# Kernel optimization log

Measured on AMD Instinct MI355X. Metric: run time of the kernel, lower is better.

The kernel has to match this reference:

```python
import jax, jax.numpy as jnp
import numpy as np


def _warp3d(img, flow):
    """Faithful port of Warper3d.forward.

    img:  [B, C, D, H, W]
    flow: [B, 3, D, H, W]  (flow[:,0]=x/W disp, flow[:,1]=y/H disp, flow[:,2]=z/D disp)

    The torch module normalizes coords align_corners=True style (2*v/(S-1)-1)
    but calls F.grid_sample with its DEFAULT align_corners=False and
    padding_mode='border'. We replicate exactly that composition.
    """
    B, C, D, H, W = img.shape
    dt = img.dtype
    zz = jnp.arange(D, dtype=dt).reshape(1, D, 1, 1)
    yy = jnp.arange(H, dtype=dt).reshape(1, 1, H, 1)
    xx = jnp.arange(W, dtype=dt).reshape(1, 1, 1, W)

    vx = xx + flow[:, 0]  # [B,D,H,W]
    vy = yy + flow[:, 1]
    vz = zz + flow[:, 2]

    # module's normalization (align_corners=True convention)
    gx = 2.0 * vx / (W - 1) - 1.0
    gy = 2.0 * vy / (H - 1) - 1.0
    gz = 2.0 * vz / (D - 1) - 1.0

    # grid_sample default align_corners=False un-normalization
    ix = ((gx + 1.0) * W - 1.0) * 0.5
    iy = ((gy + 1.0) * H - 1.0) * 0.5
    iz = ((gz + 1.0) * D - 1.0) * 0.5

    # padding_mode='border': clamp sample coords into the volume
    ix = jnp.clip(ix, 0.0, W - 1)
    iy = jnp.clip(iy, 0.0, H - 1)
    iz = jnp.clip(iz, 0.0, D - 1)

    x0f = jnp.floor(ix); wx = ix - x0f
    y0f = jnp.floor(iy); wy = iy - y0f
    z0f = jnp.floor(iz); wz = iz - z0f

    x0 = x0f.astype(jnp.int32); x1 = jnp.clip(x0 + 1, 0, W - 1)
    y0 = y0f.astype(jnp.int32); y1 = jnp.clip(y0 + 1, 0, H - 1)
    z0 = z0f.astype(jnp.int32); z1 = jnp.clip(z0 + 1, 0, D - 1)

    img_flat = img.reshape(B, C, D * H * W)

    def gather(zc, yc, xc):
        idx = (zc * H + yc) * W + xc            # [B,D,H,W]
        v = jnp.take_along_axis(img_flat, idx.reshape(B, 1, -1), axis=2)
        return v.reshape(B, C, D, H, W)

    wx = wx[:, None]; wy = wy[:, None]; wz = wz[:, None]  # [B,1,D,H,W]

    out = (
        gather(z0, y0, x0) * (1 - wz) * (1 - wy) * (1 - wx)
        + gather(z0, y0, x1) * (1 - wz) * (1 - wy) * wx
        + gather(z0, y1, x0) * (1 - wz) * wy * (1 - wx)
        + gather(z0, y1, x1) * (1 - wz) * wy * wx
        + gather(z1, y0, x0) * wz * (1 - wy) * (1 - wx)
        + gather(z1, y0, x1) * wz * (1 - wy) * wx
        + gather(z1, y1, x0) * wz * wy * (1 - wx)
        + gather(z1, y1, x1) * wz * wy * wx
    )
    return out


def setup_inputs() -> dict:
    key = jax.random.key(0)
    k1, k2 = jax.random.split(key)
    B, D, H, W = 4, 64, 192, 192
    img = jax.random.normal(k1, (B, 1, D, H, W), dtype=jnp.float32)
    flow = jax.random.normal(k2, (B, 3, D, H, W), dtype=jnp.float32)
    return {"img": img, "flow": flow}


def reference(img, flow):
    return _warp3d(img, flow)
```

## Files before the change

kernel.cpp:

```cpp
#include <hip/hip_runtime.h>

#define B_  4
#define D_  64
#define H_  192
#define W_  192
#define HW_ (H_ * W_)
#define DHW_ (D_ * H_ * W_)
#define NTOT (B_ * DHW_)
#define VEC 4
#define NTHREADS (NTOT / VEC)

typedef float f4 __attribute__((ext_vector_type(4)));
typedef float f2 __attribute__((ext_vector_type(2)));
typedef f2 f2u __attribute__((aligned(4)));

__global__ __launch_bounds__(256) void warp3d_kernel(
    const float* __restrict__ img,
    const float* __restrict__ flow,
    float* __restrict__ out)
{
    int t = blockIdx.x * blockDim.x + threadIdx.x;
    if (t >= NTHREADS) return;

    int base = t * VEC;
    int b  = base / DHW_;
    int r  = base - b * DHW_;
    int z  = r / HW_;
    int r2 = r - z * HW_;
    int y  = r2 / W_;
    int x  = r2 - y * W_;

    const float* fl = flow + (size_t)b * 3 * DHW_ + r;
    f4 fx = __builtin_nontemporal_load((const f4*)(fl));
    f4 fy = __builtin_nontemporal_load((const f4*)(fl + DHW_));
    f4 fz = __builtin_nontemporal_load((const f4*)(fl + 2 * DHW_));

    const float* im = img + (size_t)b * DHW_;

    const float sx = (float)W_ / (float)(W_ - 1);
    const float sy = (float)H_ / (float)(H_ - 1);
    const float sz = (float)D_ / (float)(D_ - 1);

    int  a00[VEC], a01[VEC], a10[VEC], a11[VEC];
    int  hi0[VEC];
    float wxv[VEC], wyv[VEC], wzv[VEC];

#pragma unroll
    for (int i = 0; i < VEC; ++i) {
        float ix = ((float)(x + i) + fx[i]) * sx - 0.5f;
        float iy = ((float)y + fy[i]) * sy - 0.5f;
        float iz = ((float)z + fz[i]) * sz - 0.5f;
        ix = fminf(fmaxf(ix, 0.0f), (float)(W_ - 1));
        iy = fminf(fmaxf(iy, 0.0f), (float)(H_ - 1));
        iz = fminf(fmaxf(iz, 0.0f), (float)(D_ - 1));

        float x0f = floorf(ix), y0f = floorf(iy), z0f = floorf(iz);
        wxv[i] = ix - x0f;
        wyv[i] = iy - y0f;
        wzv[i] = iz - z0f;

        int x0 = (int)x0f, y0 = (int)y0f, z0 = (int)z0f;
        int y1 = min(y0 + 1, H_ - 1);
        int z1 = min(z0 + 1, D_ - 1);
        int xb = min(x0, W_ - 2);
        hi0[i] = x0 - xb;

        int bz0 = z0 * HW_, bz1 = z1 * HW_;
        a00[i] = bz0 + y0 * W_ + xb;
        a01[i] = bz0 + y1 * W_ + xb;
        a10[i] = bz1 + y0 * W_ + xb;
        a11[i] = bz1 + y1 * W_ + xb;
    }

    f2 p00[VEC], p01[VEC], p10[VEC], p11[VEC];
#pragma unroll
    for (int i = 0; i < VEC; ++i) {
        p00[i] = *(const f2u*)(im + a00[i]);
        p01[i] = *(const f2u*)(im + a01[i]);
        p10[i] = *(const f2u*)(im + a10[i]);
        p11[i] = *(const f2u*)(im + a11[i]);
    }

    f4 res;
#pragma unroll
    for (int i = 0; i < VEC; ++i) {
        bool hi = (hi0[i] != 0);
        float v000 = hi ? p00[i].y : p00[i].x;
        float v010 = hi ? p01[i].y : p01[i].x;
        float v100 = hi ? p10[i].y : p10[i].x;
        float v110 = hi ? p11[i].y : p11[i].x;
        float v001 = p00[i].y;
        float v011 = p01[i].y;
        float v101 = p10[i].y;
        float v111 = p11[i].y;

        float wx = wxv[i], wy = wyv[i], wz = wzv[i];
        float c00 = v000 + wx * (v001 - v000);
        float c01 = v010 + wx * (v011 - v010);
        float c10 = v100 + wx * (v101 - v100);
        float c11 = v110 + wx * (v111 - v110);
        float c0 = c00 + wy * (c01 - c00);
        float c1 = c10 + wy * (c11 - c10);
        res[i] = c0 + wz * (c1 - c0);
    }
    __builtin_nontemporal_store(res, (f4*)(out + base));
}

extern "C" void kernel_launch(void* const* d_in, const int* in_sizes, int n_in,
                              void* d_out, int out_size, void* d_ws, size_t ws_size,
                              hipStream_t stream) {
    const float* img  = (const float*)d_in[0];
    const float* flow = (const float*)d_in[1];
    float* out = (float*)d_out;

    const int threads = 256;
    const int blocks = (NTHREADS + threads - 1) / threads;
    warp3d_kernel<<<blocks, threads, 0, stream>>>(img, flow, out);
}
```

Before: 222.6 us.

## Stage image tile with halo in LDS and gather trilinear corners from shared memory

Each workgroup now owns a 2x8 slab of full-width rows. It first copies a 10-plane by 16-row halo region of the image into LDS, then does the trilinear gather from LDS. Samples whose corners fall outside the staged halo fall back to global loads. This trades random global gathers for coalesced bulk loads, but it reads about five times more image data per output, uses a 120KB LDS buffer that limits occupancy to one 768-thread block per CU, and adds a barrier.

```diff
diff --git a/kernel.cpp b/kernel.cpp
--- a/kernel.cpp
+++ b/kernel.cpp
@@ -7,42 +7,74 @@
 #define HW_ (H_ * W_)
 #define DHW_ (D_ * H_ * W_)
 #define NTOT (B_ * DHW_)
+
+#define TY 8
+#define TZ 2
+#define SY (TY + 8)
+#define SZ (TZ + 8)
+#define SPLANE (SY * W_)
+#define SLDS (SZ * SPLANE)
+#define TILE_OUT (W_ * TY * TZ)
 #define VEC 4
-#define NTHREADS (NTOT / VEC)
+#define TPB (TILE_OUT / VEC)
+#define NWG_Y (H_ / TY)
+#define NWG_Z (D_ / TZ)
+#define NWG (B_ * NWG_Z * NWG_Y)
 
 typedef float f4 __attribute__((ext_vector_type(4)));
 typedef float f2 __attribute__((ext_vector_type(2)));
 typedef f2 f2u __attribute__((aligned(4)));
 
-__global__ __launch_bounds__(256) void warp3d_kernel(
+__global__ __launch_bounds__(TPB, 1) void warp3d_kernel(
     const float* __restrict__ img,
     const float* __restrict__ flow,
     float* __restrict__ out)
 {
-    int t = blockIdx.x * blockDim.x + threadIdx.x;
-    if (t >= NTHREADS) return;
+    __shared__ float lds[SLDS];
 
-    int base = t * VEC;
-    int b  = base / DHW_;
-    int r  = base - b * DHW_;
-    int z  = r / HW_;
-    int r2 = r - z * HW_;
-    int y  = r2 / W_;
-    int x  = r2 - y * W_;
+    int wg = blockIdx.x;
+    int b  = wg / (NWG_Z * NWG_Y);
+    int rr = wg - b * (NWG_Z * NWG_Y);
+    int tz = rr / NWG_Y;
+    int Z  = tz * TZ;
+    int Y  = (rr - tz * NWG_Y) * TY;
+    int Zs = min(max(Z - 4, 0), D_ - SZ);
+    int Ys = min(max(Y - 4, 0), H_ - SY);
 
-    const float* fl = flow + (size_t)b * 3 * DHW_ + r;
-    f4 fx = __builtin_nontemporal_load((const f4*)(fl));
+    const float* im = img + (size_t)b * DHW_;
+    int t = threadIdx.x;
+
+    {
+        int yy = (t * 4) / W_;
+        int xs = (t * 4) - yy * W_;
+        const float* src = im + (Ys + yy) * W_ + xs;
+#pragma unroll
+        for (int j = 0; j < SZ; ++j) {
+            f4 v = *(const f4*)(src + (size_t)(Zs + j) * HW_);
+            *(f4*)(lds + j * SPLANE + t * 4) = v;
+        }
+    }
+    __syncthreads();
+
+    int o  = t * VEC;
+    int x  = o % W_;
+    int q  = o / W_;
+    int yi = q % TY;
+    int zi = q / TY;
+    int y  = Y + yi;
+    int z  = Z + zi;
+
+    size_t nbase = (size_t)b * DHW_ + ((size_t)z * H_ + y) * W_ + x;
+    const float* fl = flow + (size_t)b * 3 * DHW_ + ((size_t)z * H_ + y) * W_ + x;
+    f4 fx = __builtin_nontemporal_load((const f4*)fl);
     f4 fy = __builtin_nontemporal_load((const f4*)(fl + DHW_));
     f4 fz = __builtin_nontemporal_load((const f4*)(fl + 2 * DHW_));
-
-    const float* im = img + (size_t)b * DHW_;
 
     const float sx = (float)W_ / (float)(W_ - 1);
     const float sy = (float)H_ / (float)(H_ - 1);
     const float sz = (float)D_ / (float)(D_ - 1);
 
-    int  a00[VEC], a01[VEC], a10[VEC], a11[VEC];
-    int  hi0[VEC];
+    int   xb[VEC], y0a[VEC], z0a[VEC], hi[VEC], val[VEC];
     float wxv[VEC], wyv[VEC], wzv[VEC];
 
 #pragma unroll
@@ -60,39 +92,44 @@
         wzv[i] = iz - z0f;
 
         int x0 = (int)x0f, y0 = (int)y0f, z0 = (int)z0f;
+        int xbi = min(x0, W_ - 2);
+        xb[i] = xbi;
+        hi[i] = x0 - xbi;
+        y0a[i] = y0;
+        z0a[i] = z0;
         int y1 = min(y0 + 1, H_ - 1);
         int z1 = min(z0 + 1, D_ - 1);
-        int xb = min(x0, W_ - 2);
-        hi0[i] = x0 - xb;
-
-        int bz0 = z0 * HW_, bz1 = z1 * HW_;
-        a00[i] = bz0 + y0 * W_ + xb;
-        a01[i] = bz0 + y1 * W_ + xb;
-        a10[i] = bz1 + y0 * W_ + xb;
-        a11[i] = bz1 + y1 * W_ + xb;
-    }
-
-    f2 p00[VEC], p01[VEC], p10[VEC], p11[VEC];
-#pragma unroll
-    for (int i = 0; i < VEC; ++i) {
-        p00[i] = *(const f2u*)(im + a00[i]);
-        p01[i] = *(const f2u*)(im + a01[i]);
-        p10[i] = *(const f2u*)(im + a10[i]);
-        p11[i] = *(const f2u*)(im + a11[i]);
+        val[i] = (y0 >= Ys) & (y1 <= Ys + SY - 1) &
+                 (z0 >= Zs) & (z1 <= Zs + SZ - 1);
     }
 
     f4 res;
 #pragma unroll
     for (int i = 0; i < VEC; ++i) {
-        bool hi = (hi0[i] != 0);
-        float v000 = hi ? p00[i].y : p00[i].x;
-        float v010 = hi ? p01[i].y : p01[i].x;
-        float v100 = hi ? p10[i].y : p10[i].x;
-        float v110 = hi ? p11[i].y : p11[i].x;
-        float v001 = p00[i].y;
-        float v011 = p01[i].y;
-        float v101 = p10[i].y;
-        float v111 = p11[i].y;
+        int y0 = y0a[i], z0 = z0a[i];
+        int y1 = min(y0 + 1, H_ - 1);
+        int z1 = min(z0 + 1, D_ - 1);
+        float v000, v001, v010, v011, v100, v101, v110, v111;
+        if (val[i]) {
+            int i00 = ((z0 - Zs) * SY + (y0 - Ys)) * W_ + xb[i];
+            int i01 = ((z0 - Zs) * SY + (y1 - Ys)) * W_ + xb[i];
+            int i10 = ((z1 - Zs) * SY + (y0 - Ys)) * W_ + xb[i];
+            int i11 = ((z1 - Zs) * SY + (y1 - Ys)) * W_ + xb[i];
+            v000 = lds[i00]; v001 = lds[i00 + 1];
+            v010 = lds[i01]; v011 = lds[i01 + 1];
+            v100 = lds[i10]; v101 = lds[i10 + 1];
+            v110 = lds[i11]; v111 = lds[i11 + 1];
+        } else {
+            f2 p00 = *(const f2u*)(im + (z0 * H_ + y0) * W_ + xb[i]);
+            f2 p01 = *(const f2u*)(im + (z0 * H_ + y1) * W_ + xb[i]);
+            f2 p10 = *(const f2u*)(im + (z1 * H_ + y0) * W_ + xb[i]);
+            f2 p11 = *(const f2u*)(im + (z1 * H_ + y1) * W_ + xb[i]);
+            v000 = p00.x; v001 = p00.y;
+            v010 = p01.x; v011 = p01.y;
+            v100 = p10.x; v101 = p10.y;
+            v110 = p11.x; v111 = p11.y;
+        }
+        if (hi[i]) { v000 = v001; v010 = v011; v100 = v101; v110 = v111; }
 
         float wx = wxv[i], wy = wyv[i], wz = wzv[i];
         float c00 = v000 + wx * (v001 - v000);
@@ -103,7 +140,7 @@
         float c1 = c10 + wy * (c11 - c10);
         res[i] = c0 + wz * (c1 - c0);
     }
-    __builtin_nontemporal_store(res, (f4*)(out + base));
+    __builtin_nontemporal_store(res, (f4*)(out + nbase));
 }
 
 extern "C" void kernel_launch(void* const* d_in, const int* in_sizes, int n_in,
@@ -113,7 +150,5 @@
     const float* flow = (const float*)d_in[1];
     float* out = (float*)d_out;
 
-    const int threads = 256;
-    const int blocks = (NTHREADS + threads - 1) / threads;
-    warp3d_kernel<<<blocks, threads, 0, stream>>>(img, flow, out);
+    warp3d_kernel<<<NWG, TPB, 0, stream>>>(img, flow, out);
 }
```

After: 216.0 us. -3.0%, faster.
